# Optimization experiments

Measured on AMD Instinct MI355X. Metric: run time of the kernel, lower is better.

Reference implementation:

```python
import jax, jax.numpy as jnp
import numpy as np

D_MODEL = 768
MIMO_RANK = 4


def setup_inputs() -> dict:
    key = jax.random.key(0)
    ks = jax.random.split(key, 6)
    B, T, D, R = 2, 2048, D_MODEL, MIMO_RANK
    x = jax.random.normal(ks[0], (B, T, D), dtype=jnp.float32)
    norm_w = jnp.ones((D,), dtype=jnp.float32)
    W_in = jax.random.normal(ks[1], (D * R * 2, D), dtype=jnp.float32) * 0.02
    W_out = jax.random.normal(ks[2], (D, D), dtype=jnp.float32) * 0.02
    a_param = jax.random.normal(ks[3], (D, R, 2), dtype=jnp.float32) * 0.12
    b_param = jax.random.normal(ks[4], (D, R, 2), dtype=jnp.float32) * 0.15
    c_param = jax.random.normal(ks[5], (D, R, 2), dtype=jnp.float32) * 0.15
    return {"x": x, "norm_w": norm_w, "W_in": W_in, "W_out": W_out,
            "a_param": a_param, "b_param": b_param, "c_param": c_param}


def reference(x, norm_w, W_in, W_out, a_param, b_param, c_param):
    B, T, D = x.shape
    R = a_param.shape[1]
    # RMSNorm
    xn = x * jax.lax.rsqrt(jnp.mean(x * x, axis=-1, keepdims=True) + 1e-6) * norm_w
    # in_proj -> interleaved complex MIMO input u: [B,T,D,R,2]
    u = (xn @ W_in.T).reshape(B, T, D, R, 2)
    # coefficients (tanh-bounded; |a| scaled by 0.97 for stability)
    a = jnp.tanh(a_param) * 0.97
    b = jnp.tanh(b_param)
    c = jnp.tanh(c_param)
    ac = jax.lax.complex(a[..., 0], a[..., 1])  # [D,R]
    bc = jax.lax.complex(b[..., 0], b[..., 1])
    cc = jax.lax.complex(c[..., 0], c[..., 1])
    uc = jax.lax.complex(u[..., 0], u[..., 1])  # [B,T,D,R]
    # linear complex recurrence s_t = a * s_{t-1} + b * u_t, zero init state,
    # parallelized with an associative scan over time.
    bu = bc[None, None] * uc
    A = jnp.broadcast_to(ac[None, None], bu.shape)

    def comb(l, r):
        return (l[0] * r[0], r[0] * l[1] + r[1])

    _, s = jax.lax.associative_scan(comb, (A, bu), axis=1)  # [B,T,D,R] complex
    # output mix: real part of c * h, summed over MIMO rank -> [B,T,D]
    y = jnp.real(cc[None, None] * s).sum(axis=-1)
    return y @ W_out.T
```

## Files before the change

kernel.cpp:

```cpp
#include <hip/hip_runtime.h>
#include <hip/hip_bf16.h>
#include <stdint.h>

#define BATCH 2
#define TT 2048
#define DM 768
#define RR 4
#define M_TOK 4096
#define NFEAT 6144
#define NCH 6144
#define CHUNK 64
#define NCHUNK 32

typedef __attribute__((ext_vector_type(8))) short short8;
typedef __attribute__((ext_vector_type(4))) float float4v;

__device__ inline float bf2f(uint32_t bits16) {
    union { uint32_t u; float f; } x; x.u = bits16 << 16; return x.f;
}

typedef const __attribute__((address_space(1))) void* gptr_t;
typedef __attribute__((address_space(3))) void* lptr_t;

__device__ inline void async_ld16(const void* g, void* l) {
    __builtin_amdgcn_global_load_lds((gptr_t)(uintptr_t)g, (lptr_t)(uintptr_t)l,
                                     16, 0, 0);
}

__device__ inline void store_c(__hip_bfloat16* C, size_t idx, float v) {
    C[idx] = __float2bfloat16(v);
}
__device__ inline void store_c(float* C, size_t idx, float v) { C[idx] = v; }

__device__ inline uint2 pack4bf(float a, float b, float c, float d) {
    union { __hip_bfloat16 h[4]; uint2 u; } o;
    o.h[0] = __float2bfloat16(a); o.h[1] = __float2bfloat16(b);
    o.h[2] = __float2bfloat16(c); o.h[3] = __float2bfloat16(d);
    return o.u;
}

__device__ inline float2 cmul(float2 a, float2 b) {
    return make_float2(a.x * b.x - a.y * b.y, a.x * b.y + a.y * b.x);
}
__device__ inline float2 cmad(float2 a, float2 b, float2 c) {
    return make_float2(a.x * b.x - a.y * b.y + c.x,
                       a.x * b.y + a.y * b.x + c.y);
}
__device__ inline float2 csq(float2 a) {
    return make_float2(a.x * a.x - a.y * a.y, 2.f * a.x * a.y);
}

__device__ inline void cstep(float& sr, float& si, float2 a, float2 bb,
                             uint32_t uw) {
    float ur = bf2f(uw & 0xffffu), ui = bf2f(uw >> 16);
    float tr = bb.x * ur - bb.y * ui;
    float ti = bb.x * ui + bb.y * ur;
    float nr = a.x * sr - a.y * si + tr;
    float ni = a.x * si + a.y * sr + ti;
    sr = nr; si = ni;
}

__global__ __launch_bounds__(256) void prep_rms(
    const float* __restrict__ x, const float* __restrict__ w,
    const float* __restrict__ W_in, const float* __restrict__ W_out,
    const float* __restrict__ ap, const float* __restrict__ bp,
    const float* __restrict__ cp,
    __hip_bfloat16* __restrict__ xn,
    __hip_bfloat16* __restrict__ Win_bf, __hip_bfloat16* __restrict__ Wout_bf,
    float2* __restrict__ ac, float2* __restrict__ bc,
    float2* __restrict__ cc, float2* __restrict__ aL) {
    int bid = blockIdx.x;
    int tid = threadIdx.x;
    if (bid < M_TOK) {
        __shared__ float wsum[3];
        float4 v = make_float4(0.f, 0.f, 0.f, 0.f);
        if (tid < 192) v = ((const float4*)(x + (size_t)bid * DM))[tid];
        float ss = v.x * v.x + v.y * v.y + v.z * v.z + v.w * v.w;
        #pragma unroll
        for (int o = 1; o < 64; o <<= 1) ss += __shfl_xor(ss, o);
        if (tid < 192 && (tid & 63) == 0) wsum[tid >> 6] = ss;
        __syncthreads();
        if (tid < 192) {
            float tot = wsum[0] + wsum[1] + wsum[2];
            float scale = rsqrtf(tot * (1.f / DM) + 1e-6f);
            float4 wv = ((const float4*)w)[tid];
            ((uint2*)(xn + (size_t)bid * DM))[tid] =
                pack4bf(v.x * scale * wv.x, v.y * scale * wv.y,
                        v.z * scale * wv.z, v.w * scale * wv.w);
        }
        return;
    }
    const int N1 = NFEAT * DM / 4;
    const int N2 = DM * DM / 4;
    int i = (bid - M_TOK) * 256 + tid;
    if (i < N1) {
        float4 v = ((const float4*)W_in)[i];
        ((uint2*)Win_bf)[i] = pack4bf(v.x, v.y, v.z, v.w);
    } else if (i < N1 + N2) {
        int k = i - N1;
        float4 v = ((const float4*)W_out)[k];
        ((uint2*)Wout_bf)[k] = pack4bf(v.x, v.y, v.z, v.w);
    }
    if (i < DM * RR) {
        float ar = tanhf(ap[2 * i])     * 0.97f;
        float ai = tanhf(ap[2 * i + 1]) * 0.97f;
        ac[i] = make_float2(ar, ai);
        bc[i] = make_float2(tanhf(bp[2 * i]), tanhf(bp[2 * i + 1]));
        cc[i] = make_float2(tanhf(cp[2 * i]), tanhf(cp[2 * i + 1]));
        float xr = ar, xi = ai;
        #pragma unroll
        for (int k = 0; k < 6; ++k) {
            float nr = xr * xr - xi * xi;
            float ni = 2.f * xr * xi;
            xr = nr; xi = ni;
        }
        aL[i] = make_float2(xr, xi);
    }
}

template <int BM, int BN, int BK, typename OutT>
__device__ inline void gemm_body(
    const __hip_bfloat16* __restrict__ A, const __hip_bfloat16* __restrict__ B,
    OutT* __restrict__ C, int K, int ldc) {
    constexpr int MI = BM / 32;
    constexpr int NJ = BN / 32;
    constexpr int CPR = BK / 8;
    __shared__ __attribute__((aligned(16))) __hip_bfloat16 lA[BM * BK];
    __shared__ __attribute__((aligned(16))) __hip_bfloat16 lB[BN * BK];
    const int tid  = threadIdx.x;
    const int lane = tid & 63;
    const int wave = tid >> 6;
    const int quad = lane >> 4;
    const int l15  = lane & 15;
    const int wm = (wave >> 1) * (BM / 2);
    const int wn = (wave & 1) * (BN / 2);
    const int m0 = blockIdx.y * BM;
    const int n0 = blockIdx.x * BN;

    float4v acc[MI][NJ] = {};

    for (int k0 = 0; k0 < K; k0 += BK) {
        __syncthreads();
        #pragma unroll
        for (int it = 0; it < BM * CPR / 256; ++it) {
            int p = it * 256 + tid;
            int row = p / CPR;
            int cg = (p & (CPR - 1)) ^ (row & (CPR - 1));
            async_ld16(A + (size_t)(m0 + row) * K + k0 + cg * 8, lA + p * 8);
        }
        #pragma unroll
        for (int it = 0; it < BN * CPR / 256; ++it) {
            int p = it * 256 + tid;
            int row = p / CPR;
            int cg = (p & (CPR - 1)) ^ (row & (CPR - 1));
            async_ld16(B + (size_t)(n0 + row) * K + k0 + cg * 8, lB + p * 8);
        }
        __syncthreads();
        #pragma unroll
        for (int s = 0; s < BK / 32; ++s) {
            short8 af[MI], bfr[NJ];
            #pragma unroll
            for (int i = 0; i < MI; ++i) {
                int r = wm + i * 16 + l15;
                int c = (s * 4 + quad) ^ (r & (CPR - 1));
                af[i] = *(const short8*)(lA + r * BK + c * 8);
            }
            #pragma unroll
            for (int j = 0; j < NJ; ++j) {
                int r = wn + j * 16 + l15;
                int c = (s * 4 + quad) ^ (r & (CPR - 1));
                bfr[j] = *(const short8*)(lB + r * BK + c * 8);
            }
            #pragma unroll
            for (int i = 0; i < MI; ++i)
                #pragma unroll
                for (int j = 0; j < NJ; ++j)
                    acc[i][j] = __builtin_amdgcn_mfma_f32_16x16x32_bf16(
                        af[i], bfr[j], acc[i][j], 0, 0, 0);
        }
    }
    #pragma unroll
    for (int i = 0; i < MI; ++i)
        #pragma unroll
        for (int j = 0; j < NJ; ++j)
            #pragma unroll
            for (int rg = 0; rg < 4; ++rg) {
                int row = m0 + wm + i * 16 + quad * 4 + rg;
                int col = n0 + wn + j * 16 + l15;
                store_c(C, (size_t)row * ldc + col, acc[i][j][rg]);
            }
}

__global__ __launch_bounds__(512, 4) void gemm_in(
    const __hip_bfloat16* __restrict__ A, const __hip_bfloat16* __restrict__ B,
    __hip_bfloat16* __restrict__ C, int K) {
    constexpr int BM = 128, BN = 128, BK = 64;
    constexpr int CPR = BK / 8;
    constexpr int ldc = NFEAT;
    __shared__ __attribute__((aligned(16))) __hip_bfloat16
        lds2[2][BM * BK + BN * BK];
    const int tid  = threadIdx.x;
    const int lane = tid & 63;
    const int wave = tid >> 6;
    const int quad = lane >> 4;
    const int l15  = lane & 15;
    const int wm = (wave >> 2) * 64;
    const int wn = (wave & 3) * 32;
    const int m0 = blockIdx.y * BM;
    const int n0 = blockIdx.x * BN;

    float4v acc[4][2] = {};

    auto stage = [&](int bi, int t) {
        __hip_bfloat16* sA = lds2[bi];
        __hip_bfloat16* sB = lds2[bi] + BM * BK;
        const int k0 = t * BK;
        #pragma unroll
        for (int it = 0; it < BM * CPR / 512; ++it) {
            int p = it * 512 + tid;
            int row = p >> 3;
            int cg = (p & 7) ^ (row & 7);
            async_ld16(A + (size_t)(m0 + row) * K + k0 + cg * 8, sA + p * 8);
        }
        #pragma unroll
        for (int it = 0; it < BN * CPR / 512; ++it) {
            int p = it * 512 + tid;
            int row = p >> 3;
            int cg = (p & 7) ^ (row & 7);
            async_ld16(B + (size_t)(n0 + row) * K + k0 + cg * 8, sB + p * 8);
        }
    };

    const int nt = K / BK;
    stage(0, 0);
    for (int t = 0; t < nt; ++t) {
        const int cur = t & 1;
        if (t + 1 < nt) {
            stage(cur ^ 1, t + 1);
            asm volatile("s_waitcnt vmcnt(4)" ::: "memory");
        } else {
            asm volatile("s_waitcnt vmcnt(0)" ::: "memory");
        }
        asm volatile("s_barrier" ::: "memory");
        const __hip_bfloat16* lA = lds2[cur];
        const __hip_bfloat16* lB = lds2[cur] + BM * BK;
        #pragma unroll
        for (int s = 0; s < BK / 32; ++s) {
            short8 af[4], bfr[2];
            #pragma unroll
            for (int i = 0; i < 4; ++i) {
                int r = wm + i * 16 + l15;
                int c = (s * 4 + quad) ^ (r & 7);
                af[i] = *(const short8*)(lA + r * BK + c * 8);
            }
            #pragma unroll
            for (int j = 0; j < 2; ++j) {
                int r = wn + j * 16 + l15;
                int c = (s * 4 + quad) ^ (r & 7);
                bfr[j] = *(const short8*)(lB + r * BK + c * 8);
            }
            #pragma unroll
            for (int i = 0; i < 4; ++i)
                #pragma unroll
                for (int j = 0; j < 2; ++j)
                    acc[i][j] = __builtin_amdgcn_mfma_f32_16x16x32_bf16(
                        af[i], bfr[j], acc[i][j], 0, 0, 0);
        }
        asm volatile("s_waitcnt lgkmcnt(0)" ::: "memory");
        asm volatile("s_barrier" ::: "memory");
    }
    #pragma unroll
    for (int i = 0; i < 4; ++i)
        #pragma unroll
        for (int j = 0; j < 2; ++j)
            #pragma unroll
            for (int rg = 0; rg < 4; ++rg) {
                int row = m0 + wm + i * 16 + quad * 4 + rg;
                int col = n0 + wn + j * 16 + l15;
                C[(size_t)row * ldc + col] = __float2bfloat16(acc[i][j][rg]);
            }
}

__global__ __launch_bounds__(256) void gemm_out(
    const __hip_bfloat16* __restrict__ A, const __hip_bfloat16* __restrict__ B,
    float* __restrict__ C, int K) {
    gemm_body<64, 64, 128, float>(A, B, C, K, DM);
}

__global__ __launch_bounds__(256) void scan_local2(
    const uint4* __restrict__ u4,
    const float2* __restrict__ ac, const float2* __restrict__ bc,
    const float2* __restrict__ cc,
    __hip_bfloat16* __restrict__ y_local,
    float2* __restrict__ chunkEnd) {
    __shared__ float2 se[1024];
    const int tid   = threadIdx.x;
    const int d_loc = tid & 31;
    const int s8    = tid >> 5;
    const int bd    = blockIdx.x;
    const int b     = bd >= 24;
    const int dg    = bd - b * 24;
    const int d_g   = dg * 32 + d_loc;
    const int cb    = d_g * RR;
    const int j     = blockIdx.y;

    float2 a0 = ac[cb], a1 = ac[cb + 1], a2 = ac[cb + 2], a3 = ac[cb + 3];
    float2 b0 = bc[cb], b1 = bc[cb + 1], b2 = bc[cb + 2], b3 = bc[cb + 3];
    float2 c0 = cc[cb], c1 = cc[cb + 1], c2 = cc[cb + 2], c3 = cc[cb + 3];

    const int token0 = b * TT + j * CHUNK + s8 * 8;
    const size_t base = (size_t)token0 * DM + d_g;

    uint4 uw[8];
    #pragma unroll
    for (int i = 0; i < 8; ++i) uw[i] = u4[base + (size_t)i * DM];
    float s0r = 0, s0i = 0, s1r = 0, s1i = 0;
    float s2r = 0, s2i = 0, s3r = 0, s3i = 0;
    float yloc[8];
    #pragma unroll
    for (int i = 0; i < 8; ++i) {
        cstep(s0r, s0i, a0, b0, uw[i].x);
        cstep(s1r, s1i, a1, b1, uw[i].y);
        cstep(s2r, s2i, a2, b2, uw[i].z);
        cstep(s3r, s3i, a3, b3, uw[i].w);
        yloc[i] = c0.x * s0r - c0.y * s0i + c1.x * s1r - c1.y * s1i
                + c2.x * s2r - c2.y * s2i + c3.x * s3r - c3.y * s3i;
    }
    se[tid * 4]     = make_float2(s0r, s0i);
    se[tid * 4 + 1] = make_float2(s1r, s1i);
    se[tid * 4 + 2] = make_float2(s2r, s2i);
    se[tid * 4 + 3] = make_float2(s3r, s3i);
    __syncthreads();

    float2 aE0 = csq(csq(csq(a0))), aE1 = csq(csq(csq(a1)));
    float2 aE2 = csq(csq(csq(a2))), aE3 = csq(csq(csq(a3)));
    float2 C0 = make_float2(0, 0), C1 = C0, C2 = C0, C3 = C0;
    for (int k = 0; k < s8; ++k) {
        int kb = (k * 32 + d_loc) * 4;
        C0 = cmad(C0, aE0, se[kb]);
        C1 = cmad(C1, aE1, se[kb + 1]);
        C2 = cmad(C2, aE2, se[kb + 2]);
        C3 = cmad(C3, aE3, se[kb + 3]);
    }
    if (s8 == 7) {
        size_t eb = (size_t)j * NCH + b * (DM * RR) + cb;
        chunkEnd[eb]     = cmad(C0, aE0, make_float2(s0r, s0i));
        chunkEnd[eb + 1] = cmad(C1, aE1, make_float2(s1r, s1i));
        chunkEnd[eb + 2] = cmad(C2, aE2, make_float2(s2r, s2i));
        chunkEnd[eb + 3] = cmad(C3, aE3, make_float2(s3r, s3i));
    }
    float2 q0 = cmul(cmul(c0, C0), a0);
    float2 q1 = cmul(cmul(c1, C1), a1);
    float2 q2 = cmul(cmul(c2, C2), a2);
    float2 q3 = cmul(cmul(c3, C3), a3);
    #pragma unroll
    for (int i = 0; i < 8; ++i) {
        float yv = yloc[i] + q0.x + q1.x + q2.x + q3.x;
        y_local[base + (size_t)i * DM] = __float2bfloat16(yv);
        q0 = cmul(q0, a0); q1 = cmul(q1, a1);
        q2 = cmul(q2, a2); q3 = cmul(q3, a3);
    }
}

__global__ __launch_bounds__(256) void carry_scan(
    float2* __restrict__ chunkEnd,
    const float2* __restrict__ aLp) {
    int ch = blockIdx.x * 256 + threadIdx.x;
    int dr = (ch >= DM * RR) ? ch - DM * RR : ch;
    float2 aL = aLp[dr];
    float2 K = make_float2(0.f, 0.f);
    for (int j = 0; j < NCHUNK; ++j) {
        size_t idx = (size_t)j * NCH + ch;
        float2 e = chunkEnd[idx];
        chunkEnd[idx] = K;
        K = cmad(K, aL, e);
    }
}

__global__ __launch_bounds__(256) void scan_fix(
    __hip_bfloat16* __restrict__ y_local,
    const float2* __restrict__ ac, const float2* __restrict__ cc,
    const float2* __restrict__ carry) {
    const int tid   = threadIdx.x;
    const int d_loc = tid & 31;
    const int s8    = tid >> 5;
    const int bd    = blockIdx.x;
    const int b     = bd >= 24;
    const int dg    = bd - b * 24;
    const int d_g   = dg * 32 + d_loc;
    const int cb    = d_g * RR;
    const int j     = blockIdx.y;
    const size_t kb = (size_t)j * NCH + b * (DM * RR) + cb;

    float2 a0 = ac[cb], a1 = ac[cb + 1], a2 = ac[cb + 2], a3 = ac[cb + 3];
    float2 c0 = cc[cb], c1 = cc[cb + 1], c2 = cc[cb + 2], c3 = cc[cb + 3];
    float2 K0 = carry[kb],     K1 = carry[kb + 1];
    float2 K2 = carry[kb + 2], K3 = carry[kb + 3];

    float2 aE0 = csq(csq(csq(a0))), aE1 = csq(csq(csq(a1)));
    float2 aE2 = csq(csq(csq(a2))), aE3 = csq(csq(csq(a3)));
    float2 q0 = cmul(cmul(c0, K0), a0);
    float2 q1 = cmul(cmul(c1, K1), a1);
    float2 q2 = cmul(cmul(c2, K2), a2);
    float2 q3 = cmul(cmul(c3, K3), a3);
    for (int t = 0; t < s8; ++t) {
        q0 = cmul(q0, aE0); q1 = cmul(q1, aE1);
        q2 = cmul(q2, aE2); q3 = cmul(q3, aE3);
    }
    const int token0 = b * TT + j * CHUNK + s8 * 8;
    const size_t base = (size_t)token0 * DM + d_g;
    #pragma unroll
    for (int i = 0; i < 8; ++i) {
        size_t idx = base + (size_t)i * DM;
        float yv = bf2f(((const uint16_t*)y_local)[idx])
                 + q0.x + q1.x + q2.x + q3.x;
        y_local[idx] = __float2bfloat16(yv);
        q0 = cmul(q0, a0); q1 = cmul(q1, a1);
        q2 = cmul(q2, a2); q3 = cmul(q3, a3);
    }
}

extern "C" void kernel_launch(void* const* d_in, const int* in_sizes, int n_in,
                              void* d_out, int out_size, void* d_ws,
                              size_t ws_size, hipStream_t stream) {
    const float* x      = (const float*)d_in[0];
    const float* norm_w = (const float*)d_in[1];
    const float* W_in   = (const float*)d_in[2];
    const float* W_out  = (const float*)d_in[3];
    const float* a_p    = (const float*)d_in[4];
    const float* b_p    = (const float*)d_in[5];
    const float* c_p    = (const float*)d_in[6];
    float* out = (float*)d_out;

    char* ws = (char*)d_ws;
    size_t off = 0;
    auto alloc = [&](size_t bytes) {
        void* p = ws + off;
        off += (bytes + 255) & ~(size_t)255;
        return p;
    };
    __hip_bfloat16* Win_bf  = (__hip_bfloat16*)alloc((size_t)NFEAT * DM * 2);
    __hip_bfloat16* Wout_bf = (__hip_bfloat16*)alloc((size_t)DM * DM * 2);
    __hip_bfloat16* xn      = (__hip_bfloat16*)alloc((size_t)M_TOK * DM * 2);
    __hip_bfloat16* u       = (__hip_bfloat16*)alloc((size_t)M_TOK * NFEAT * 2);
    __hip_bfloat16* y_local = (__hip_bfloat16*)alloc((size_t)M_TOK * DM * 2);
    float2* ac = (float2*)alloc((size_t)DM * RR * 8);
    float2* bc = (float2*)alloc((size_t)DM * RR * 8);
    float2* cc = (float2*)alloc((size_t)DM * RR * 8);
    float2* aL = (float2*)alloc((size_t)DM * RR * 8);
    float2* chunkEnd = (float2*)alloc((size_t)NCHUNK * NCH * 8);

    {
        int cast_blocks = ((NFEAT * DM + DM * DM) / 4 + 255) / 256;
        prep_rms<<<M_TOK + cast_blocks, 256, 0, stream>>>(
            x, norm_w, W_in, W_out, a_p, b_p, c_p,
            xn, Win_bf, Wout_bf, ac, bc, cc, aL);
    }
    gemm_in<<<dim3(NFEAT / 128, M_TOK / 128), 512, 0, stream>>>(
        xn, Win_bf, u, DM);
    scan_local2<<<dim3(48, NCHUNK), 256, 0, stream>>>(
        (const uint4*)u, ac, bc, cc, y_local, chunkEnd);
    carry_scan<<<NCH / 256, 256, 0, stream>>>(chunkEnd, aL);
    scan_fix<<<dim3(48, NCHUNK), 256, 0, stream>>>(
        y_local, ac, cc, chunkEnd);
    gemm_out<<<dim3(DM / 64, M_TOK / 64), 256, 0, stream>>>(
        y_local, Wout_bf, out, DM);
}
```

Before: 170.6 us.

## Fuse carry scan into scan_fix and restructure prep RMS and cast blocks

Removes the separate carry_scan kernel. Each scan_fix block now recomputes its incoming chunk carry by serially folding the previous chunk-end states into shared memory, which trades redundant work for one fewer launch and round trip. The RMSNorm path now handles one token per wavefront, four tokens per block, with no shared-memory barrier. The weight cast uses a fixed grid in which each thread converts four elements with a strided loop, which cuts the number of launched blocks.

```diff
diff --git a/kernel.cpp b/kernel.cpp
--- a/kernel.cpp
+++ b/kernel.cpp
@@ -60,6 +60,8 @@
     sr = nr; si = ni;
 }
 
+#define RMS_BLOCKS (M_TOK / 4)
+#define CAST_BLOCKS 1296
 __global__ __launch_bounds__(256) void prep_rms(
     const float* __restrict__ x, const float* __restrict__ w,
     const float* __restrict__ W_in, const float* __restrict__ W_out,
@@ -71,37 +73,46 @@
     float2* __restrict__ cc, float2* __restrict__ aL) {
     int bid = blockIdx.x;
     int tid = threadIdx.x;
-    if (bid < M_TOK) {
-        __shared__ float wsum[3];
-        float4 v = make_float4(0.f, 0.f, 0.f, 0.f);
-        if (tid < 192) v = ((const float4*)(x + (size_t)bid * DM))[tid];
-        float ss = v.x * v.x + v.y * v.y + v.z * v.z + v.w * v.w;
+    if (bid < RMS_BLOCKS) {
+        int lane = tid & 63;
+        int token = bid * 4 + (tid >> 6);
+        const float4* xr = (const float4*)(x + (size_t)token * DM);
+        float4 v0 = xr[lane], v1 = xr[lane + 64], v2 = xr[lane + 128];
+        float ss = v0.x * v0.x + v0.y * v0.y + v0.z * v0.z + v0.w * v0.w
+                 + v1.x * v1.x + v1.y * v1.y + v1.z * v1.z + v1.w * v1.w
+                 + v2.x * v2.x + v2.y * v2.y + v2.z * v2.z + v2.w * v2.w;
         #pragma unroll
         for (int o = 1; o < 64; o <<= 1) ss += __shfl_xor(ss, o);
-        if (tid < 192 && (tid & 63) == 0) wsum[tid >> 6] = ss;
-        __syncthreads();
-        if (tid < 192) {
-            float tot = wsum[0] + wsum[1] + wsum[2];
-            float scale = rsqrtf(tot * (1.f / DM) + 1e-6f);
-            float4 wv = ((const float4*)w)[tid];
-            ((uint2*)(xn + (size_t)bid * DM))[tid] =
-                pack4bf(v.x * scale * wv.x, v.y * scale * wv.y,
-                        v.z * scale * wv.z, v.w * scale * wv.w);
-        }
+        float scale = rsqrtf(ss * (1.f / DM) + 1e-6f);
+        const float4* wr = (const float4*)w;
+        float4 w0 = wr[lane], w1 = wr[lane + 64], w2 = wr[lane + 128];
+        uint2* o = (uint2*)(xn + (size_t)token * DM);
+        o[lane] = pack4bf(v0.x * scale * w0.x, v0.y * scale * w0.y,
+                          v0.z * scale * w0.z, v0.w * scale * w0.w);
+        o[lane + 64] = pack4bf(v1.x * scale * w1.x, v1.y * scale * w1.y,
+                               v1.z * scale * w1.z, v1.w * scale * w1.w);
+        o[lane + 128] = pack4bf(v2.x * scale * w2.x, v2.y * scale * w2.y,
+                                v2.z * scale * w2.z, v2.w * scale * w2.w);
         return;
     }
     const int N1 = NFEAT * DM / 4;
     const int N2 = DM * DM / 4;
-    int i = (bid - M_TOK) * 256 + tid;
-    if (i < N1) {
-        float4 v = ((const float4*)W_in)[i];
-        ((uint2*)Win_bf)[i] = pack4bf(v.x, v.y, v.z, v.w);
-    } else if (i < N1 + N2) {
-        int k = i - N1;
-        float4 v = ((const float4*)W_out)[k];
-        ((uint2*)Wout_bf)[k] = pack4bf(v.x, v.y, v.z, v.w);
-    }
-    if (i < DM * RR) {
+    const int STR = CAST_BLOCKS * 256;
+    int gid = (bid - RMS_BLOCKS) * 256 + tid;
+    #pragma unroll
+    for (int k = 0; k < 4; ++k) {
+        int i = gid + k * STR;
+        if (i < N1) {
+            float4 v = ((const float4*)W_in)[i];
+            ((uint2*)Win_bf)[i] = pack4bf(v.x, v.y, v.z, v.w);
+        } else if (i < N1 + N2) {
+            int kk = i - N1;
+            float4 v = ((const float4*)W_out)[kk];
+            ((uint2*)Wout_bf)[kk] = pack4bf(v.x, v.y, v.z, v.w);
+        }
+    }
+    if (gid < DM * RR) {
+        int i = gid;
         float ar = tanhf(ap[2 * i])     * 0.97f;
         float ai = tanhf(ap[2 * i + 1]) * 0.97f;
         ac[i] = make_float2(ar, ai);
@@ -362,40 +373,38 @@
     }
 }
 
-__global__ __launch_bounds__(256) void carry_scan(
-    float2* __restrict__ chunkEnd,
-    const float2* __restrict__ aLp) {
-    int ch = blockIdx.x * 256 + threadIdx.x;
-    int dr = (ch >= DM * RR) ? ch - DM * RR : ch;
-    float2 aL = aLp[dr];
-    float2 K = make_float2(0.f, 0.f);
-    for (int j = 0; j < NCHUNK; ++j) {
-        size_t idx = (size_t)j * NCH + ch;
-        float2 e = chunkEnd[idx];
-        chunkEnd[idx] = K;
-        K = cmad(K, aL, e);
-    }
-}
-
 __global__ __launch_bounds__(256) void scan_fix(
     __hip_bfloat16* __restrict__ y_local,
     const float2* __restrict__ ac, const float2* __restrict__ cc,
-    const float2* __restrict__ carry) {
+    const float2* __restrict__ aLp,
+    const float2* __restrict__ chunkEnd) {
+    __shared__ float2 ksh[128];
     const int tid   = threadIdx.x;
-    const int d_loc = tid & 31;
-    const int s8    = tid >> 5;
     const int bd    = blockIdx.x;
     const int b     = bd >= 24;
     const int dg    = bd - b * 24;
+    const int j     = blockIdx.y;
+
+    if (tid < 128) {
+        const int dl = tid >> 2;
+        const int r  = tid & 3;
+        const int ch = (dg * 32 + dl) * RR + r;
+        float2 aL = aLp[ch];
+        float2 K = make_float2(0.f, 0.f);
+        for (int jj = 0; jj < j; ++jj)
+            K = cmad(K, aL, chunkEnd[(size_t)jj * NCH + b * (DM * RR) + ch]);
+        ksh[tid] = K;
+    }
+    __syncthreads();
+
+    const int d_loc = tid & 31;
+    const int s8    = tid >> 5;
     const int d_g   = dg * 32 + d_loc;
     const int cb    = d_g * RR;
-    const int j     = blockIdx.y;
-    const size_t kb = (size_t)j * NCH + b * (DM * RR) + cb;
-
     float2 a0 = ac[cb], a1 = ac[cb + 1], a2 = ac[cb + 2], a3 = ac[cb + 3];
     float2 c0 = cc[cb], c1 = cc[cb + 1], c2 = cc[cb + 2], c3 = cc[cb + 3];
-    float2 K0 = carry[kb],     K1 = carry[kb + 1];
-    float2 K2 = carry[kb + 2], K3 = carry[kb + 3];
+    float2 K0 = ksh[d_loc * 4],     K1 = ksh[d_loc * 4 + 1];
+    float2 K2 = ksh[d_loc * 4 + 2], K3 = ksh[d_loc * 4 + 3];
 
     float2 aE0 = csq(csq(csq(a0))), aE1 = csq(csq(csq(a1)));
     float2 aE2 = csq(csq(csq(a2))), aE3 = csq(csq(csq(a3)));
@@ -450,19 +459,15 @@
     float2* aL = (float2*)alloc((size_t)DM * RR * 8);
     float2* chunkEnd = (float2*)alloc((size_t)NCHUNK * NCH * 8);
 
-    {
-        int cast_blocks = ((NFEAT * DM + DM * DM) / 4 + 255) / 256;
-        prep_rms<<<M_TOK + cast_blocks, 256, 0, stream>>>(
-            x, norm_w, W_in, W_out, a_p, b_p, c_p,
-            xn, Win_bf, Wout_bf, ac, bc, cc, aL);
-    }
+    prep_rms<<<RMS_BLOCKS + CAST_BLOCKS, 256, 0, stream>>>(
+        x, norm_w, W_in, W_out, a_p, b_p, c_p,
+        xn, Win_bf, Wout_bf, ac, bc, cc, aL);
     gemm_in<<<dim3(NFEAT / 128, M_TOK / 128), 512, 0, stream>>>(
         xn, Win_bf, u, DM);
     scan_local2<<<dim3(48, NCHUNK), 256, 0, stream>>>(
         (const uint4*)u, ac, bc, cc, y_local, chunkEnd);
-    carry_scan<<<NCH / 256, 256, 0, stream>>>(chunkEnd, aL);
     scan_fix<<<dim3(48, NCHUNK), 256, 0, stream>>>(
-        y_local, ac, cc, chunkEnd);
+        y_local, ac, cc, aL, chunkEnd);
     gemm_out<<<dim3(DM / 64, M_TOK / 64), 256, 0, stream>>>(
         y_local, Wout_bf, out, DM);
 }
```

New measurement: 172.3 us. About the same (+1.0%).
